# Kernel tuning notes

Measured on AMD Instinct MI355X. Metric: run time of the kernel, lower is better.

Reference implementation:

```python
import jax, jax.numpy as jnp
import numpy as np
import math

N_HEADS = 8
FACTOR = 5       # ProbSparse factor from DistSparseAtt(False, 5, ...)
LN_EPS = 1e-5


def _layer_norm(x, g, b):
    mu = x.mean(-1, keepdims=True)
    var = ((x - mu) ** 2).mean(-1, keepdims=True)
    return (x - mu) / jnp.sqrt(var + LN_EPS) * g + b


def _prob_sparse_attention(Q, K, V):
    # Informer-style ProbSparse attention, mask_flag=False, eval mode (no dropout).
    # Q, K, V: [B, H, L, Dh]
    B, H, L, Dh = Q.shape
    u = min(int(FACTOR * math.ceil(math.log(L))), L)  # sample_k == n_top (L_Q == L_K)
    # deterministic key sampling (torch.randint in the original)
    idx = jax.random.randint(jax.random.key(42), (L, u), 0, L)  # [L, u]
    K_samp = K[:, :, idx, :]                                    # [B,H,L,u,Dh]
    qk = jnp.einsum('bhld,bhlsd->bhls', Q, K_samp)              # [B,H,L,u]
    M = qk.max(-1) - qk.mean(-1)                                # sparsity measure [B,H,L]
    _, top = jax.lax.top_k(M, u)                                # [B,H,u] top-query indices
    Q_red = jnp.take_along_axis(Q, top[..., None], axis=2)      # [B,H,u,Dh]
    scale = 1.0 / jnp.sqrt(jnp.asarray(Dh, Q.dtype))
    scores = jnp.einsum('bhud,bhld->bhul', Q_red, K) * scale    # [B,H,u,L]
    attn = jax.nn.softmax(scores, axis=-1)
    upd = jnp.einsum('bhul,bhld->bhud', attn, V)                # [B,H,u,Dh]
    # initial context = mean of V over keys (mask_flag=False branch)
    ctx0 = jnp.broadcast_to(V.mean(axis=2, keepdims=True), Q.shape)
    ctx = jax.vmap(jax.vmap(lambda c, i, w: c.at[i].set(w)))(ctx0, top, upd)
    return ctx                                                  # [B,H,L,Dh]


def setup_inputs() -> dict:
    key = jax.random.key(0)
    ks = jax.random.split(key, 8)
    L, B, D, DFF = 1024, 4, 768, 2048
    return {
        'target': jax.random.normal(ks[0], (L, B, D), jnp.float32),
        'source': jax.random.normal(ks[1], (L, B, D), jnp.float32),
        'W1': jax.random.normal(ks[2], (DFF, D), jnp.float32) * 0.02,
        'b1': jax.random.normal(ks[3], (DFF,), jnp.float32) * 0.02,
        'W2': jax.random.normal(ks[4], (D, DFF), jnp.float32) * 0.02,
        'b2': jax.random.normal(ks[5], (D,), jnp.float32) * 0.02,
        'ln1_g': jnp.ones((D,), jnp.float32),
        'ln1_b': jnp.zeros((D,), jnp.float32),
        'ln2_g': jnp.ones((D,), jnp.float32),
        'ln2_b': jnp.zeros((D,), jnp.float32),
    }


def reference(target, source, W1, b1, W2, b2, ln1_g, ln1_b, ln2_g, ln2_b):
    L, B, Dm = target.shape
    Dh = Dm // N_HEADS
    # [L,B,Dm] -> [B,H,L,Dh]
    Q = jnp.transpose(target.reshape(L, B, N_HEADS, Dh), (1, 2, 0, 3))
    K = jnp.transpose(source.reshape(L, B, N_HEADS, Dh), (1, 2, 0, 3))
    ctx = _prob_sparse_attention(Q, K, K)                 # [B,H,L,Dh]
    attended = jnp.transpose(ctx, (2, 0, 1, 3)).reshape(L, B, Dm)
    normed1 = _layer_norm(target + attended, ln1_g, ln1_b)
    proj = jax.nn.relu(normed1 @ W1.T + b1) @ W2.T + b2
    return _layer_norm(normed1 + proj, ln2_g, ln2_b)
```

## Files before the change

kernel.cpp:

```cpp
#include <hip/hip_runtime.h>
#include <hip/hip_bf16.h>
#include <math.h>

#define L_SEQ 1024
#define BATCH 4
#define DMODEL 768
#define NH 8
#define DH 96
#define DFF 2048
#define U_TOP 35
#define NROWS (L_SEQ * BATCH)
#define NBH (BATCH * NH)
#define IDX_CNT (L_SEQ * U_TOP)
#define CHUNK 64
#define NCHUNK (L_SEQ / CHUNK)
#define VCH 64

typedef __attribute__((ext_vector_type(8))) short bf16x8;
typedef __attribute__((ext_vector_type(4))) float f32x4;

__device__ inline unsigned short f2bf(float f) {
  unsigned u = __float_as_uint(f);
  u += 0x7FFFu + ((u >> 16) & 1u);
  return (unsigned short)(u >> 16);
}

__device__ inline unsigned rotl32(unsigned v, int d) { return (v << d) | (v >> (32 - d)); }

__device__ inline void tf2x32(unsigned k0, unsigned k1, unsigned x0, unsigned x1,
                              unsigned& o0, unsigned& o1) {
  unsigned ks0 = k0, ks1 = k1, ks2 = k0 ^ k1 ^ 0x1BD11BDAu;
  x0 += ks0; x1 += ks1;
#define TFR(r) { x0 += x1; x1 = rotl32(x1, r); x1 ^= x0; }
  TFR(13) TFR(15) TFR(26) TFR(6)
  x0 += ks1; x1 += ks2 + 1u;
  TFR(17) TFR(29) TFR(16) TFR(24)
  x0 += ks2; x1 += ks0 + 2u;
  TFR(13) TFR(15) TFR(26) TFR(6)
  x0 += ks0; x1 += ks1 + 3u;
  TFR(17) TFR(29) TFR(16) TFR(24)
  x0 += ks1; x1 += ks2 + 4u;
  TFR(13) TFR(15) TFR(26) TFR(6)
  x0 += ks2; x1 += ks0 + 5u;
#undef TFR
  o0 = x0; o1 = x1;
}

__global__ void gen_idx(int* __restrict__ idx) {
  int j = blockIdx.x * 256 + threadIdx.x;
  if (j >= IDX_CNT) return;
  unsigned k2a, k2b;
  tf2x32(0u, 42u, 0u, 1u, k2a, k2b);
  unsigned o0, o1;
  tf2x32(k2a, k2b, 0u, (unsigned)j, o0, o1);
  idx[j] = (int)((o0 ^ o1) & 1023u);
}

__global__ __launch_bounds__(256) void sample_scores(
    const float* __restrict__ target, const float* __restrict__ source,
    const int* __restrict__ idx, float* __restrict__ M) {
  int orig = blockIdx.x;
  int blk = (orig & 7) * (BATCH * L_SEQ / 8) + (orig >> 3);
  int l = blk & (L_SEQ - 1);
  int b = blk >> 10;
  __shared__ float qkbuf[NH][40];
  __shared__ int sidx[40];
  int tid = threadIdx.x;
  if (tid < 40) sidx[tid] = (tid < U_TOP) ? idx[l * U_TOP + tid] : 0;
  int h = (tid >> 2) & 7, p = tid & 3;
  int s8 = tid >> 5;
  float4 qreg[6];
  {
    const float4* qg = (const float4*)(target + ((size_t)l * BATCH + b) * DMODEL + h * DH + p * 24);
#pragma unroll
    for (int j = 0; j < 6; ++j) qreg[j] = qg[j];
  }
  __syncthreads();
#pragma unroll
  for (int c = 0; c < 5; ++c) {
    int s = c * 8 + s8;
    if (s < U_TOP) {
      int kl = sidx[s];
      const float4* kg = (const float4*)(source + ((size_t)kl * BATCH + b) * DMODEL + h * DH + p * 24);
      float a = 0.f;
#pragma unroll
      for (int j = 0; j < 6; ++j) {
        float4 kv = kg[j];
        float4 qv = qreg[j];
        a += qv.x * kv.x + qv.y * kv.y + qv.z * kv.z + qv.w * kv.w;
      }
      a += __shfl_xor(a, 1, 64);
      a += __shfl_xor(a, 2, 64);
      if (p == 0) qkbuf[h][s] = a;
    }
  }
  __syncthreads();
  int w = tid >> 6, lane = tid & 63;
#pragma unroll
  for (int hi = 0; hi < 2; ++hi) {
    int hh = w * 2 + hi;
    float v = (lane < U_TOP) ? qkbuf[hh][lane] : -INFINITY;
    float sm = (lane < U_TOP) ? v : 0.f;
    float mx = v;
#pragma unroll
    for (int off = 32; off; off >>= 1) {
      mx = fmaxf(mx, __shfl_xor(mx, off, 64));
      sm += __shfl_xor(sm, off, 64);
    }
    if (lane == 0)
      M[(size_t)(b * NH + hh) * L_SEQ + l] = mx - sm * (1.f / U_TOP);
  }
}

__global__ __launch_bounds__(256) void topk_sel(const float* __restrict__ M,
                                                int* __restrict__ top, int* __restrict__ sel) {
  int bh = blockIdx.x;
  int tid = threadIdx.x;
  int lane = tid & 63, w = tid >> 6;
  __shared__ float wval[4];
  __shared__ int widx[4];
  __shared__ int bidx_sh;
  float v[4]; int ir[4];
#pragma unroll
  for (int i = 0; i < 4; ++i) {
    int ii = tid + i * 256;
    v[i] = M[(size_t)bh * L_SEQ + ii];
    ir[i] = ii;
    sel[(size_t)bh * L_SEQ + ii] = -1;
  }
  for (int it = 0; it < U_TOP; ++it) {
    float bv = v[0]; int bi = ir[0];
#pragma unroll
    for (int i = 1; i < 4; ++i)
      if (v[i] > bv || (v[i] == bv && ir[i] < bi)) { bv = v[i]; bi = ir[i]; }
#pragma unroll
    for (int off = 32; off; off >>= 1) {
      float ov = __shfl_xor(bv, off, 64);
      int oi = __shfl_xor(bi, off, 64);
      if (ov > bv || (ov == bv && oi < bi)) { bv = ov; bi = oi; }
    }
    if (lane == 0) { wval[w] = bv; widx[w] = bi; }
    __syncthreads();
    if (tid == 0) {
      float fv = wval[0]; int fi = widx[0];
#pragma unroll
      for (int k = 1; k < 4; ++k)
        if (wval[k] > fv || (wval[k] == fv && widx[k] < fi)) { fv = wval[k]; fi = widx[k]; }
      top[bh * U_TOP + it] = fi;
      sel[(size_t)bh * L_SEQ + fi] = it;
      bidx_sh = fi;
    }
    __syncthreads();
    int rb = bidx_sh;
    if ((rb & 255) == tid) v[rb >> 8] = -INFINITY;
  }
}

__global__ __launch_bounds__(768) void vmean_part(const float* __restrict__ source,
                                                  float* __restrict__ part) {
  int blk = blockIdx.x;
  int b = blk >> 6, c = blk & (VCH - 1);
  int d = threadIdx.x;
  float s = 0.f;
  int l0 = c * (L_SEQ / VCH);
#pragma unroll
  for (int l = l0; l < l0 + L_SEQ / VCH; ++l)
    s += source[((size_t)l * BATCH + b) * DMODEL + d];
  part[(size_t)blk * DMODEL + d] = s;
}

__global__ __launch_bounds__(768) void vmean_comb(const float* __restrict__ part,
                                                  float* __restrict__ vmean) {
  int b = blockIdx.x;
  int d = threadIdx.x;
  float s = 0.f;
  for (int c = 0; c < VCH; ++c) s += part[((size_t)(b * VCH + c)) * DMODEL + d];
  vmean[b * DMODEL + d] = s * (1.f / L_SEQ);
}

__global__ __launch_bounds__(256) void attn_flash(
    const float* __restrict__ target, const float* __restrict__ source,
    const int* __restrict__ top,
    float* __restrict__ part_O,
    float* __restrict__ part_m,
    float* __restrict__ part_s) {
  int blk = blockIdx.x;
  int chunk = blk & (NCHUNK - 1);
  int bh = blk >> 4;
  int h = bh & (NH - 1), b = bh >> 3;
  __shared__ short Qb[48 * 104];
  __shared__ short Kb[CHUNK * 104];
  __shared__ short Vt[96 * 72];
  __shared__ float sc[48 * 66];
  int tid = threadIdx.x;
  const float scale = 0.1020620726f;
  for (int i = tid; i < 13 * 104; i += 256) Qb[35 * 104 + i] = 0;
  for (int i = tid; i < U_TOP * 24; i += 256) {
    int u = i / 24, d4 = i - u * 24;
    int qpos = top[bh * U_TOP + u];
    float4 v = *(const float4*)(target + ((size_t)qpos * BATCH + b) * DMODEL + h * DH + d4 * 4);
    short* dst = Qb + u * 104 + d4 * 4;
    dst[0] = f2bf(v.x * scale); dst[1] = f2bf(v.y * scale);
    dst[2] = f2bf(v.z * scale); dst[3] = f2bf(v.w * scale);
  }
  int l0 = chunk * CHUNK;
  for (int i = tid; i < CHUNK * 24; i += 256) {
    int r = i / 24, d4 = i - r * 24;
    float4 v = *(const float4*)(source + ((size_t)(l0 + r) * BATCH + b) * DMODEL + h * DH + d4 * 4);
    short* dst = Kb + r * 104 + d4 * 4;
    dst[0] = f2bf(v.x); dst[1] = f2bf(v.y); dst[2] = f2bf(v.z); dst[3] = f2bf(v.w);
  }
  __syncthreads();
  for (int i = tid; i < CHUNK * 24; i += 256) {
    int r = i & (CHUNK - 1), d4 = i >> 6;
    const short* srcp = Kb + r * 104 + d4 * 4;
#pragma unroll
    for (int cc = 0; cc < 4; ++cc) Vt[(d4 * 4 + cc) * 72 + r] = srcp[cc];
  }
  int wv = tid >> 6, lane = tid & 63;
  int lr = lane & 15, lg = lane >> 4;
  __syncthreads();
  {
    int n = wv;
#pragma unroll
    for (int m = 0; m < 3; ++m) {
      f32x4 acc = {};
#pragma unroll
      for (int kc = 0; kc < 3; ++kc) {
        bf16x8 a = *(const bf16x8*)(Qb + (m * 16 + lr) * 104 + kc * 32 + lg * 8);
        bf16x8 bb = *(const bf16x8*)(Kb + (n * 16 + lr) * 104 + kc * 32 + lg * 8);
        acc = __builtin_amdgcn_mfma_f32_16x16x32_bf16(a, bb, acc, 0, 0, 0);
      }
#pragma unroll
      for (int j = 0; j < 4; ++j)
        sc[(m * 16 + lg * 4 + j) * 66 + n * 16 + lr] = acc[j];
    }
  }
  __syncthreads();
#pragma unroll
  for (int i = 0; i < 9; ++i) {
    int u = wv + 4 * i;
    if (u < U_TOP) {
      float s = sc[u * 66 + lane];
      float mx = s;
#pragma unroll
      for (int off = 32; off; off >>= 1) mx = fmaxf(mx, __shfl_xor(mx, off, 64));
      float pp = expf(s - mx);
      float sm = pp;
#pragma unroll
      for (int off = 32; off; off >>= 1) sm += __shfl_xor(sm, off, 64);
      Qb[u * 104 + lane] = f2bf(pp);
      if (lane == 0) {
        part_m[blk * U_TOP + u] = mx;
        part_s[blk * U_TOP + u] = sm;
      }
    }
  }
  __syncthreads();
  for (int t = wv; t < 18; t += 4) {
    int m = t / 6, n = t - (t / 6) * 6;
    f32x4 acc = {};
#pragma unroll
    for (int kc = 0; kc < 2; ++kc) {
      bf16x8 a = *(const bf16x8*)(Qb + (m * 16 + lr) * 104 + kc * 32 + lg * 8);
      bf16x8 bb = *(const bf16x8*)(Vt + (n * 16 + lr) * 72 + kc * 32 + lg * 8);
      acc = __builtin_amdgcn_mfma_f32_16x16x32_bf16(a, bb, acc, 0, 0, 0);
    }
#pragma unroll
    for (int j = 0; j < 4; ++j) {
      int u = m * 16 + lg * 4 + j;
      if (u < U_TOP)
        part_O[(size_t)blk * U_TOP * DH + u * DH + n * 16 + lr] = acc[j];
    }
  }
}

__global__ __launch_bounds__(256) void attn_combine(
    const float* __restrict__ part_O, const float* __restrict__ part_m,
    const float* __restrict__ part_s, float* __restrict__ upd) {
  int bh = blockIdx.x;
  __shared__ float w[NCHUNK][U_TOP];
  __shared__ float Sinv[U_TOP];
  int tid = threadIdx.x;
  if (tid < U_TOP) {
    float m = -INFINITY;
    for (int c = 0; c < NCHUNK; ++c)
      m = fmaxf(m, part_m[(bh * NCHUNK + c) * U_TOP + tid]);
    float s = 0.f;
    for (int c = 0; c < NCHUNK; ++c) {
      float wv = expf(part_m[(bh * NCHUNK + c) * U_TOP + tid] - m);
      w[c][tid] = wv;
      s += wv * part_s[(bh * NCHUNK + c) * U_TOP + tid];
    }
    Sinv[tid] = 1.f / s;
  }
  __syncthreads();
  for (int i = tid; i < U_TOP * DH; i += 256) {
    int u = i / DH;
    float acc = 0.f;
#pragma unroll
    for (int c = 0; c < NCHUNK; ++c)
      acc += w[c][u] * part_O[((size_t)bh * NCHUNK + c) * U_TOP * DH + i];
    upd[(size_t)bh * U_TOP * DH + i] = acc * Sinv[u];
  }
}

__global__ __launch_bounds__(256) void fuse_ln1(
    const float* __restrict__ target, const float* __restrict__ upd,
    const int* __restrict__ sel, const float* __restrict__ vmean,
    const float* __restrict__ g, const float* __restrict__ bb,
    float* __restrict__ normed1, unsigned short* __restrict__ normed1b) {
  int r = blockIdx.x;
  int l = r >> 2, b = r & 3;
  __shared__ float x[DMODEL];
  __shared__ float red[256];
  int tid = threadIdx.x;
  for (int d = tid; d < DMODEL; d += 256) {
    int h = d / DH;
    int s = sel[((size_t)(b * NH + h)) * L_SEQ + l];
    float a = (s >= 0) ? upd[((size_t)(b * NH + h) * U_TOP + s) * DH + (d - h * DH)]
                       : vmean[b * DMODEL + d];
    x[d] = target[(size_t)r * DMODEL + d] + a;
  }
  __syncthreads();
  float partial = 0.f;
  for (int d = tid; d < DMODEL; d += 256) partial += x[d];
  red[tid] = partial; __syncthreads();
  for (int s = 128; s; s >>= 1) { if (tid < s) red[tid] += red[tid + s]; __syncthreads(); }
  float mu = red[0] * (1.f / DMODEL);
  __syncthreads();
  partial = 0.f;
  for (int d = tid; d < DMODEL; d += 256) { float t = x[d] - mu; partial += t * t; }
  red[tid] = partial; __syncthreads();
  for (int s = 128; s; s >>= 1) { if (tid < s) red[tid] += red[tid + s]; __syncthreads(); }
  float rstd = 1.0f / sqrtf(red[0] * (1.f / DMODEL) + 1e-5f);
  for (int d = tid; d < DMODEL; d += 256) {
    float v = (x[d] - mu) * rstd * g[d] + bb[d];
    normed1[(size_t)r * DMODEL + d] = v;
    normed1b[(size_t)r * DMODEL + d] = f2bf(v);
  }
}

__global__ __launch_bounds__(256) void convert_bf16(const float* __restrict__ in,
                                                    unsigned short* __restrict__ outp, int n4) {
  int i = blockIdx.x * 256 + threadIdx.x;
  int stride = gridDim.x * 256;
  for (; i < n4; i += stride) {
    float4 v = ((const float4*)in)[i];
    unsigned long long pk = (unsigned long long)f2bf(v.x)
                          | ((unsigned long long)f2bf(v.y) << 16)
                          | ((unsigned long long)f2bf(v.z) << 32)
                          | ((unsigned long long)f2bf(v.w) << 48);
    ((unsigned long long*)outp)[i] = pk;
  }
}

template <bool RELU, bool BF16OUT>
__global__ __launch_bounds__(256) void gemm_mfma64(
    const unsigned short* __restrict__ A, const unsigned short* __restrict__ B,
    const float* __restrict__ bias, void* __restrict__ Cout,
    int Ndim, int Kdim) {
  __shared__ short As[64 * 64];
  __shared__ short Bs[64 * 64];
  int tid = threadIdx.x;
  int lane = tid & 63;
  int wid = tid >> 6;
  int wm = wid >> 1, wn = wid & 1;
  int bm = blockIdx.y * 64, bn = blockIdx.x * 64;

  f32x4 acc[2][2] = {};

  for (int k0 = 0; k0 < Kdim; k0 += 64) {
#pragma unroll
    for (int i = 0; i < 2; ++i) {
      int trow = wid * 16 + i * 8 + (lane >> 3);
      int slot = (lane & 7) ^ (trow & 7);
      const unsigned short* ga = A + (size_t)(bm + trow) * Kdim + k0 + slot * 8;
      const unsigned short* gb = B + (size_t)(bn + trow) * Kdim + k0 + slot * 8;
      __builtin_amdgcn_global_load_lds(
          (const __attribute__((address_space(1))) void*)ga,
          (__attribute__((address_space(3))) void*)(As + (wid * 16 + i * 8) * 64),
          16, 0, 0);
      __builtin_amdgcn_global_load_lds(
          (const __attribute__((address_space(1))) void*)gb,
          (__attribute__((address_space(3))) void*)(Bs + (wid * 16 + i * 8) * 64),
          16, 0, 0);
    }
    __syncthreads();
#pragma unroll
    for (int c = 0; c < 2; ++c) {
      bf16x8 af[2], bf[2];
#pragma unroll
      for (int mi = 0; mi < 2; ++mi) {
        int row = wm * 32 + mi * 16 + (lane & 15);
        int phys = (c * 4 + (lane >> 4)) ^ (row & 7);
        af[mi] = *(const bf16x8*)(As + row * 64 + phys * 8);
      }
#pragma unroll
      for (int ni = 0; ni < 2; ++ni) {
        int row = wn * 32 + ni * 16 + (lane & 15);
        int phys = (c * 4 + (lane >> 4)) ^ (row & 7);
        bf[ni] = *(const bf16x8*)(Bs + row * 64 + phys * 8);
      }
#pragma unroll
      for (int mi = 0; mi < 2; ++mi)
#pragma unroll
        for (int ni = 0; ni < 2; ++ni)
          acc[mi][ni] = __builtin_amdgcn_mfma_f32_16x16x32_bf16(af[mi], bf[ni], acc[mi][ni], 0, 0, 0);
    }
    __syncthreads();
  }

#pragma unroll
  for (int mi = 0; mi < 2; ++mi)
#pragma unroll
    for (int ni = 0; ni < 2; ++ni) {
      int col = bn + wn * 32 + ni * 16 + (lane & 15);
      float bv = bias[col];
#pragma unroll
      for (int j = 0; j < 4; ++j) {
        int row = bm + wm * 32 + mi * 16 + (lane >> 4) * 4 + j;
        float v = acc[mi][ni][j] + bv;
        if (RELU) v = fmaxf(v, 0.f);
        if (BF16OUT)
          ((unsigned short*)Cout)[(size_t)row * Ndim + col] = f2bf(v);
        else
          ((float*)Cout)[(size_t)row * Ndim + col] = v;
      }
    }
}

__global__ __launch_bounds__(192) void ln2_out(
    const float* __restrict__ normed1, const float* __restrict__ proj,
    const float* __restrict__ g, const float* __restrict__ bb,
    float* __restrict__ out) {
  int r = blockIdx.x;
  int tid = threadIdx.x;
  __shared__ float red[6];
  float4 a = ((const float4*)(normed1 + (size_t)r * DMODEL))[tid];
  float4 p = ((const float4*)(proj + (size_t)r * DMODEL))[tid];
  float4 x = {a.x + p.x, a.y + p.y, a.z + p.z, a.w + p.w};
  float s1 = x.x + x.y + x.z + x.w;
  float s2 = x.x * x.x + x.y * x.y + x.z * x.z + x.w * x.w;
#pragma unroll
  for (int off = 32; off; off >>= 1) {
    s1 += __shfl_xor(s1, off, 64);
    s2 += __shfl_xor(s2, off, 64);
  }
  int w = tid >> 6;
  if ((tid & 63) == 0) { red[w] = s1; red[3 + w] = s2; }
  __syncthreads();
  float S1 = red[0] + red[1] + red[2];
  float S2 = red[3] + red[4] + red[5];
  float mu = S1 * (1.f / DMODEL);
  float var = S2 * (1.f / DMODEL) - mu * mu;
  float rstd = 1.0f / sqrtf(var + 1e-5f);
  float4 gv = ((const float4*)g)[tid];
  float4 bv = ((const float4*)bb)[tid];
  float4 o = {(x.x - mu) * rstd * gv.x + bv.x, (x.y - mu) * rstd * gv.y + bv.y,
              (x.z - mu) * rstd * gv.z + bv.z, (x.w - mu) * rstd * gv.w + bv.w};
  ((float4*)(out + (size_t)r * DMODEL))[tid] = o;
}

extern "C" void kernel_launch(void* const* d_in, const int* in_sizes, int n_in,
                              void* d_out, int out_size, void* d_ws, size_t ws_size,
                              hipStream_t stream) {
  const float* target = (const float*)d_in[0];
  const float* source = (const float*)d_in[1];
  const float* W1 = (const float*)d_in[2];
  const float* b1 = (const float*)d_in[3];
  const float* W2 = (const float*)d_in[4];
  const float* b2 = (const float*)d_in[5];
  const float* ln1_g = (const float*)d_in[6];
  const float* ln1_b = (const float*)d_in[7];
  const float* ln2_g = (const float*)d_in[8];
  const float* ln2_b = (const float*)d_in[9];
  float* out = (float*)d_out;

  char* ws = (char*)d_ws;
  int*            idx      = (int*)           (ws + 0x0000000);
  float*          M        = (float*)         (ws + 0x0040000);
  int*            top      = (int*)           (ws + 0x0080000);
  int*            sel      = (int*)           (ws + 0x0090000);
  float*          upd      = (float*)         (ws + 0x00C0000);
  float*          vmean    = (float*)         (ws + 0x0130000);
  float*          part_m   = (float*)         (ws + 0x0140000);
  float*          part_s   = (float*)         (ws + 0x0160000);
  unsigned short* w1b      = (unsigned short*)(ws + 0x0180000);
  unsigned short* w2b      = (unsigned short*)(ws + 0x0480000);
  unsigned short* normed1b = (unsigned short*)(ws + 0x0780000);
  float*          normed1  = (float*)         (ws + 0x0D80000);
  unsigned short* h1b      = (unsigned short*)(ws + 0x1980000);
  float*          part_O   = (float*)         (ws + 0x1980000);
  float*          vpart    = (float*)         (ws + 0x2200000);
  float*          proj     = (float*)         (ws + 0x2980000);

  gen_idx<<<(IDX_CNT + 255) / 256, 256, 0, stream>>>(idx);
  sample_scores<<<BATCH * L_SEQ, 256, 0, stream>>>(target, source, idx, M);
  topk_sel<<<NBH, 256, 0, stream>>>(M, top, sel);
  vmean_part<<<BATCH * VCH, 768, 0, stream>>>(source, vpart);
  vmean_comb<<<BATCH, 768, 0, stream>>>(vpart, vmean);
  attn_flash<<<NBH * NCHUNK, 256, 0, stream>>>(target, source, top, part_O, part_m, part_s);
  attn_combine<<<NBH, 256, 0, stream>>>(part_O, part_m, part_s, upd);
  convert_bf16<<<1024, 256, 0, stream>>>(W1, w1b, DFF * DMODEL / 4);
  convert_bf16<<<1024, 256, 0, stream>>>(W2, w2b, DFF * DMODEL / 4);
  fuse_ln1<<<NROWS, 256, 0, stream>>>(target, upd, sel, vmean, ln1_g, ln1_b, normed1, normed1b);
  {
    dim3 grid(DFF / 64, NROWS / 64);
    gemm_mfma64<true, true><<<grid, 256, 0, stream>>>(normed1b, w1b, b1, h1b, DFF, DMODEL);
  }
  {
    dim3 grid(DMODEL / 64, NROWS / 64);
    gemm_mfma64<false, false><<<grid, 256, 0, stream>>>(h1b, w2b, b2, proj, DMODEL, DFF);
  }
  ln2_out<<<NROWS, 192, 0, stream>>>(normed1, proj, ln2_g, ln2_b, out);
}
```

Before: 175.2 us.

## Fuse index generation, attention combine and weight conversions to cut kernel launches

Computes the random key-sampling indices inline in sample_scores instead of in a separate kernel, and folds the cross-chunk softmax combine into the LN1 kernel. Only rows that a selected query lands on read the partial outputs. The two weight bf16 conversions are merged into one launch. This removes three kernel launches and the round trip through the upd buffer. In exchange, the Threefry hash is recomputed per block and each selected row redoes the 16-chunk weighted reduction inside fuse_ln1.

```diff
diff --git a/kernel.cpp b/kernel.cpp
--- a/kernel.cpp
+++ b/kernel.cpp
@@ -11,7 +11,6 @@
 #define U_TOP 35
 #define NROWS (L_SEQ * BATCH)
 #define NBH (BATCH * NH)
-#define IDX_CNT (L_SEQ * U_TOP)
 #define CHUNK 64
 #define NCHUNK (L_SEQ / CHUNK)
 #define VCH 64
@@ -46,19 +45,16 @@
   o0 = x0; o1 = x1;
 }
 
-__global__ void gen_idx(int* __restrict__ idx) {
-  int j = blockIdx.x * 256 + threadIdx.x;
-  if (j >= IDX_CNT) return;
-  unsigned k2a, k2b;
+__device__ inline int jax_randint1024(int j) {
+  unsigned k2a, k2b, o0, o1;
   tf2x32(0u, 42u, 0u, 1u, k2a, k2b);
-  unsigned o0, o1;
   tf2x32(k2a, k2b, 0u, (unsigned)j, o0, o1);
-  idx[j] = (int)((o0 ^ o1) & 1023u);
+  return (int)((o0 ^ o1) & 1023u);
 }
 
 __global__ __launch_bounds__(256) void sample_scores(
     const float* __restrict__ target, const float* __restrict__ source,
-    const int* __restrict__ idx, float* __restrict__ M) {
+    float* __restrict__ M) {
   int orig = blockIdx.x;
   int blk = (orig & 7) * (BATCH * L_SEQ / 8) + (orig >> 3);
   int l = blk & (L_SEQ - 1);
@@ -66,7 +62,7 @@
   __shared__ float qkbuf[NH][40];
   __shared__ int sidx[40];
   int tid = threadIdx.x;
-  if (tid < 40) sidx[tid] = (tid < U_TOP) ? idx[l * U_TOP + tid] : 0;
+  if (tid < 40) sidx[tid] = (tid < U_TOP) ? jax_randint1024(l * U_TOP + tid) : 0;
   int h = (tid >> 2) & 7, p = tid & 3;
   int s8 = tid >> 5;
   float4 qreg[6];
@@ -275,51 +271,55 @@
   }
 }
 
-__global__ __launch_bounds__(256) void attn_combine(
-    const float* __restrict__ part_O, const float* __restrict__ part_m,
-    const float* __restrict__ part_s, float* __restrict__ upd) {
-  int bh = blockIdx.x;
-  __shared__ float w[NCHUNK][U_TOP];
-  __shared__ float Sinv[U_TOP];
-  int tid = threadIdx.x;
-  if (tid < U_TOP) {
-    float m = -INFINITY;
-    for (int c = 0; c < NCHUNK; ++c)
-      m = fmaxf(m, part_m[(bh * NCHUNK + c) * U_TOP + tid]);
-    float s = 0.f;
-    for (int c = 0; c < NCHUNK; ++c) {
-      float wv = expf(part_m[(bh * NCHUNK + c) * U_TOP + tid] - m);
-      w[c][tid] = wv;
-      s += wv * part_s[(bh * NCHUNK + c) * U_TOP + tid];
-    }
-    Sinv[tid] = 1.f / s;
-  }
-  __syncthreads();
-  for (int i = tid; i < U_TOP * DH; i += 256) {
-    int u = i / DH;
-    float acc = 0.f;
-#pragma unroll
-    for (int c = 0; c < NCHUNK; ++c)
-      acc += w[c][u] * part_O[((size_t)bh * NCHUNK + c) * U_TOP * DH + i];
-    upd[(size_t)bh * U_TOP * DH + i] = acc * Sinv[u];
-  }
-}
-
 __global__ __launch_bounds__(256) void fuse_ln1(
-    const float* __restrict__ target, const float* __restrict__ upd,
+    const float* __restrict__ target, const float* __restrict__ part_O,
+    const float* __restrict__ part_m, const float* __restrict__ part_s,
     const int* __restrict__ sel, const float* __restrict__ vmean,
     const float* __restrict__ g, const float* __restrict__ bb,
     float* __restrict__ normed1, unsigned short* __restrict__ normed1b) {
   int r = blockIdx.x;
   int l = r >> 2, b = r & 3;
+  __shared__ float wgt[NH][NCHUNK];
+  __shared__ float sinv[NH];
+  __shared__ int uarr[NH];
   __shared__ float x[DMODEL];
   __shared__ float red[256];
   int tid = threadIdx.x;
+  if (tid < NH) uarr[tid] = sel[((size_t)(b * NH + tid)) * L_SEQ + l];
+  __syncthreads();
+  if (tid < NH * NCHUNK) {
+    int h = tid >> 4, c = tid & 15;
+    int u = uarr[h];
+    if (u >= 0) {
+      int bh = b * NH + h;
+      float pm = part_m[(bh * NCHUNK + c) * U_TOP + u];
+      float mx = pm;
+#pragma unroll
+      for (int off = 1; off < 16; off <<= 1) mx = fmaxf(mx, __shfl_xor(mx, off, 64));
+      float wv = expf(pm - mx);
+      float sv = wv * part_s[(bh * NCHUNK + c) * U_TOP + u];
+#pragma unroll
+      for (int off = 1; off < 16; off <<= 1) sv += __shfl_xor(sv, off, 64);
+      wgt[h][c] = wv;
+      if (c == 0) sinv[h] = 1.f / sv;
+    }
+  }
+  __syncthreads();
   for (int d = tid; d < DMODEL; d += 256) {
     int h = d / DH;
-    int s = sel[((size_t)(b * NH + h)) * L_SEQ + l];
-    float a = (s >= 0) ? upd[((size_t)(b * NH + h) * U_TOP + s) * DH + (d - h * DH)]
-                       : vmean[b * DMODEL + d];
+    int u = uarr[h];
+    float a;
+    if (u >= 0) {
+      int bh = b * NH + h;
+      int dd = d - h * DH;
+      float acc = 0.f;
+#pragma unroll
+      for (int c = 0; c < NCHUNK; ++c)
+        acc += wgt[h][c] * part_O[((size_t)(bh * NCHUNK + c) * U_TOP + u) * DH + dd];
+      a = acc * sinv[h];
+    } else {
+      a = vmean[b * DMODEL + d];
+    }
     x[d] = target[(size_t)r * DMODEL + d] + a;
   }
   __syncthreads();
@@ -341,17 +341,21 @@
   }
 }
 
-__global__ __launch_bounds__(256) void convert_bf16(const float* __restrict__ in,
-                                                    unsigned short* __restrict__ outp, int n4) {
+__global__ __launch_bounds__(256) void convert_bf16_2(
+    const float* __restrict__ inA, const float* __restrict__ inB,
+    unsigned short* __restrict__ outA, unsigned short* __restrict__ outB, int n4each) {
   int i = blockIdx.x * 256 + threadIdx.x;
   int stride = gridDim.x * 256;
-  for (; i < n4; i += stride) {
-    float4 v = ((const float4*)in)[i];
+  for (; i < 2 * n4each; i += stride) {
+    const float* in = (i < n4each) ? inA : inB;
+    unsigned short* outp = (i < n4each) ? outA : outB;
+    int k = (i < n4each) ? i : i - n4each;
+    float4 v = ((const float4*)in)[k];
     unsigned long long pk = (unsigned long long)f2bf(v.x)
                           | ((unsigned long long)f2bf(v.y) << 16)
                           | ((unsigned long long)f2bf(v.z) << 32)
                           | ((unsigned long long)f2bf(v.w) << 48);
-    ((unsigned long long*)outp)[i] = pk;
+    ((unsigned long long*)outp)[k] = pk;
   }
 }
 
@@ -478,11 +482,9 @@
   float* out = (float*)d_out;
 
   char* ws = (char*)d_ws;
-  int*            idx      = (int*)           (ws + 0x0000000);
   float*          M        = (float*)         (ws + 0x0040000);
   int*            top      = (int*)           (ws + 0x0080000);
   int*            sel      = (int*)           (ws + 0x0090000);
-  float*          upd      = (float*)         (ws + 0x00C0000);
   float*          vmean    = (float*)         (ws + 0x0130000);
   float*          part_m   = (float*)         (ws + 0x0140000);
   float*          part_s   = (float*)         (ws + 0x0160000);
@@ -495,16 +497,14 @@
   float*          vpart    = (float*)         (ws + 0x2200000);
   float*          proj     = (float*)         (ws + 0x2980000);
 
-  gen_idx<<<(IDX_CNT + 255) / 256, 256, 0, stream>>>(idx);
-  sample_scores<<<BATCH * L_SEQ, 256, 0, stream>>>(target, source, idx, M);
+  sample_scores<<<BATCH * L_SEQ, 256, 0, stream>>>(target, source, M);
   topk_sel<<<NBH, 256, 0, stream>>>(M, top, sel);
   vmean_part<<<BATCH * VCH, 768, 0, stream>>>(source, vpart);
   vmean_comb<<<BATCH, 768, 0, stream>>>(vpart, vmean);
   attn_flash<<<NBH * NCHUNK, 256, 0, stream>>>(target, source, top, part_O, part_m, part_s);
-  attn_combine<<<NBH, 256, 0, stream>>>(part_O, part_m, part_s, upd);
-  convert_bf16<<<1024, 256, 0, stream>>>(W1, w1b, DFF * DMODEL / 4);
-  convert_bf16<<<1024, 256, 0, stream>>>(W2, w2b, DFF * DMODEL / 4);
-  fuse_ln1<<<NROWS, 256, 0, stream>>>(target, upd, sel, vmean, ln1_g, ln1_b, normed1, normed1b);
+  convert_bf16_2<<<1024, 256, 0, stream>>>(W1, W2, w1b, w2b, DFF * DMODEL / 4);
+  fuse_ln1<<<NROWS, 256, 0, stream>>>(target, part_O, part_m, part_s, sel, vmean,
+                                      ln1_g, ln1_b, normed1, normed1b);
   {
     dim3 grid(DFF / 64, NROWS / 64);
     gemm_mfma64<true, true><<<grid, 256, 0, stream>>>(normed1b, w1b, b1, h1b, DFF, DMODEL);
```

Measured after the change: 161.8 us. 7.7% less time.
